# Performance work log

Measured on AMD Instinct MI355X. Metric: run time of the kernel, lower is better.

The kernel has to match this reference:

```python
import jax, jax.numpy as jnp
import numpy as np

EMBED = 8192      # DYNAMIC(2048) + STATIC(6144)
U0, U1 = 1024, 256  # units
EGO = 3
NUM_HEAD = 6
ACTION = 2
MEAN_SCALE = 5.0
INIT_STD = 5.0
MIN_STD = 1e-4
BATCH = 8192


def setup_inputs() -> dict:
    key = jax.random.key(0)
    ks = jax.random.split(key, 10)
    s = lambda fan_in: 1.0 / np.sqrt(fan_in)
    x = jax.random.normal(ks[0], (BATCH, EMBED), dtype=jnp.float32)
    # command head index in [0, 6) == RoadOption.value - 1
    command = jax.random.randint(ks[1], (BATCH,), 0, NUM_HEAD, dtype=jnp.int32)
    ego_state = jax.random.normal(ks[2], (BATCH, EGO), dtype=jnp.float32)
    # shared trunk fc: Linear(EMBED -> U0)
    fc_W = jax.random.uniform(ks[3], (EMBED, U0), jnp.float32, -s(EMBED), s(EMBED))
    fc_b = jax.random.uniform(ks[4], (U0,), jnp.float32, -s(EMBED), s(EMBED))
    # per-head MLP: Linear(U0+EGO -> U1) -> ReLU -> Linear(U1 -> 2*ACTION)
    cin = U0 + EGO
    W1 = jax.random.uniform(ks[5], (NUM_HEAD, cin, U1), jnp.float32, -s(cin), s(cin))
    b1 = jax.random.uniform(ks[6], (NUM_HEAD, U1), jnp.float32, -s(cin), s(cin))
    W2 = jax.random.uniform(ks[7], (NUM_HEAD, U1, 2 * ACTION), jnp.float32, -s(U1), s(U1))
    b2 = jax.random.uniform(ks[8], (NUM_HEAD, 2 * ACTION), jnp.float32, -s(U1), s(U1))
    return {"x": x, "command": command, "ego_state": ego_state,
            "fc_W": fc_W, "fc_b": fc_b, "W1": W1, "b1": b1, "W2": W2, "b2": b2}


def reference(x, command, ego_state, fc_W, fc_b, W1, b1, W2, b2):
    # shared trunk: Linear + ReLU, then concat ego state -> [B, U0+EGO]
    h = jax.nn.relu(x @ fc_W + fc_b)
    h = jnp.concatenate([h, ego_state], axis=-1)
    # routed heads: compute all 6 small heads densely, then select per sample
    # (faithful math; an optimized kernel would gather->grouped GEMM->scatter)
    h1 = jax.nn.relu(jnp.einsum('bi,hio->bho', h, W1) + b1)          # [B, H, U1]
    h2 = jnp.einsum('bhi,hio->bho', h1, W2) + b2                      # [B, H, 2A]
    sel = jnp.take_along_axis(h2, command[:, None, None].astype(jnp.int32), axis=1)
    out = sel[:, 0, :]                                                # [B, 2A]
    mean, std = jnp.split(out, 2, axis=-1)
    mean = MEAN_SCALE * jnp.tanh(mean / MEAN_SCALE)
    raw_init_std = np.float32(np.log(np.exp(INIT_STD) - 1.0))
    std = jax.nn.softplus(std + raw_init_std) + MIN_STD
    # distribution parameters (pre TanhBijector Normal params)
    return jnp.concatenate([mean, std], axis=-1)
```

## Files before the change

kernel.cpp:

```cpp
#include <hip/hip_runtime.h>
#include <stdint.h>

typedef short bf16x8 __attribute__((ext_vector_type(8)));
typedef float f32x4 __attribute__((ext_vector_type(4)));

#define BATCH 8192
#define EMBED 8192
#define U0    1024
#define U1    256
#define NHEAD 6

__device__ __forceinline__ unsigned short f2bf(float f) {
  union { float f; unsigned int u; } v; v.f = f;
  unsigned int u = v.u;
  unsigned int r = u + 0x7FFFu + ((u >> 16) & 1u);
  return (unsigned short)(r >> 16);
}
__device__ __forceinline__ unsigned int pk2(float lo, float hi) {
  return (unsigned int)f2bf(lo) | ((unsigned int)f2bf(hi) << 16);
}
__device__ __forceinline__ void async_copy16(const void* g, void* l) {
  __builtin_amdgcn_global_load_lds((const __attribute__((address_space(1))) void*)g,
                                   (__attribute__((address_space(3))) void*)l, 16, 0, 0);
}

__global__ void cvt_x_kernel(const float* __restrict__ x, unsigned short* __restrict__ xb) {
  long i = ((long)blockIdx.x * 256 + threadIdx.x) * 8;
  float4 a = *(const float4*)(x + i);
  float4 b = *(const float4*)(x + i + 4);
  uint4 r;
  r.x = pk2(a.x, a.y); r.y = pk2(a.z, a.w);
  r.z = pk2(b.x, b.y); r.w = pk2(b.z, b.w);
  *(uint4*)(xb + i) = r;
}

__global__ void transpose_cvt_kernel(const float* __restrict__ in, unsigned short* __restrict__ out,
                                     int R, int C, long in_z, long out_z) {
  __shared__ unsigned short tile[64][65];
  const float* inp = in + (long)blockIdx.z * in_z;
  unsigned short* outp = out + (long)blockIdx.z * out_z;
  int r0 = blockIdx.x * 64;
  int c0 = blockIdx.y * 64;
  int lc = threadIdx.x & 63;
  int lr = threadIdx.x >> 6;
#pragma unroll
  for (int i = 0; i < 16; i++) {
    int r = lr + i * 4;
    tile[r][lc] = f2bf(inp[(long)(r0 + r) * C + (c0 + lc)]);
  }
  __syncthreads();
#pragma unroll
  for (int i = 0; i < 16; i++) {
    int c = lr + i * 4;
    outp[(long)(c0 + c) * R + (r0 + lc)] = tile[lc][c];
  }
}

__global__ void bucket_kernel(const int* __restrict__ cmd, int* __restrict__ idxlist,
                              int* __restrict__ meta) {
  __shared__ int cnt[NHEAD], cur[NHEAD], off[NHEAD + 1];
  int tid = threadIdx.x;
  if (tid < NHEAD) cnt[tid] = 0;
  __syncthreads();
  for (int b = tid; b < BATCH; b += blockDim.x) atomicAdd(&cnt[cmd[b]], 1);
  __syncthreads();
  if (tid == 0) {
    int s = 0;
    for (int h2 = 0; h2 < NHEAD; h2++) { off[h2] = s; s += cnt[h2]; }
    off[NHEAD] = s;
  }
  __syncthreads();
  if (tid < NHEAD) cur[tid] = off[tid];
  if (tid <= NHEAD) meta[tid] = off[tid];
  __syncthreads();
  for (int b = tid; b < BATCH; b += blockDim.x) {
    int p = atomicAdd(&cur[cmd[b]], 1);
    idxlist[p] = b;
  }
}

__global__ __launch_bounds__(256) void gemm_kernel(const unsigned short* __restrict__ xb,
                                                   const unsigned short* __restrict__ wt,
                                                   const float* __restrict__ fc_b,
                                                   unsigned short* __restrict__ h) {
  __shared__ uint4 As[1024];
  __shared__ uint4 Bs[1024];
  int tid  = threadIdx.x;
  int lane = tid & 63;
  int wave = tid >> 6;
  int wm = wave >> 1, wn = wave & 1;
  int m0 = blockIdx.y * 128;
  int n0 = blockIdx.x * 128;
  int l15 = lane & 15, lq = lane >> 4;

  long asrc[4], bsrc[4];
#pragma unroll
  for (int j = 0; j < 4; j++) {
    int c = wave * 4 + j;
    int cwm = c >> 3, cks = (c >> 2) & 1, cmi = c & 3;
    int kofs = cks * 32 + lq * 8;
    asrc[j] = (long)(m0 + cwm * 64 + cmi * 16 + l15) * EMBED + kofs;
    bsrc[j] = (long)(n0 + cwm * 64 + cmi * 16 + l15) * EMBED + kofs;
  }

  f32x4 zero = {0.f, 0.f, 0.f, 0.f};
  f32x4 acc[4][4];
#pragma unroll
  for (int mi = 0; mi < 4; mi++)
#pragma unroll
    for (int ni = 0; ni < 4; ni++) acc[mi][ni] = zero;

  for (int k0 = 0; k0 < EMBED; k0 += 64) {
    __syncthreads();
#pragma unroll
    for (int j = 0; j < 4; j++) {
      int c = wave * 4 + j;
      async_copy16(xb + asrc[j] + k0, &As[c * 64 + lane]);
      async_copy16(wt + bsrc[j] + k0, &Bs[c * 64 + lane]);
    }
    __syncthreads();
#pragma unroll
    for (int ks = 0; ks < 2; ks++) {
      bf16x8 af[4], bfr[4];
#pragma unroll
      for (int mi = 0; mi < 4; mi++) af[mi] = *(const bf16x8*)&As[((wm * 2 + ks) * 4 + mi) * 64 + lane];
#pragma unroll
      for (int ni = 0; ni < 4; ni++) bfr[ni] = *(const bf16x8*)&Bs[((wn * 2 + ks) * 4 + ni) * 64 + lane];
#pragma unroll
      for (int mi = 0; mi < 4; mi++)
#pragma unroll
        for (int ni = 0; ni < 4; ni++)
          acc[mi][ni] = __builtin_amdgcn_mfma_f32_16x16x32_bf16(af[mi], bfr[ni], acc[mi][ni], 0, 0, 0);
    }
  }

#pragma unroll
  for (int ni = 0; ni < 4; ni++) {
    int col = n0 + wn * 64 + ni * 16 + l15;
    float bias = fc_b[col];
#pragma unroll
    for (int mi = 0; mi < 4; mi++) {
      int rbase = m0 + wm * 64 + mi * 16 + lq * 4;
#pragma unroll
      for (int r = 0; r < 4; r++) {
        float v = acc[mi][ni][r] + bias;
        v = v > 0.f ? v : 0.f;
        h[(long)(rbase + r) * U0 + col] = f2bf(v);
      }
    }
  }
}

__global__ __launch_bounds__(256) void head_kernel(const unsigned short* __restrict__ h,
                                                   const unsigned short* __restrict__ w1t,
                                                   const float* __restrict__ W1,
                                                   const float* __restrict__ b1,
                                                   const float* __restrict__ W2,
                                                   const float* __restrict__ b2,
                                                   const float* __restrict__ ego,
                                                   const int* __restrict__ idxlist,
                                                   const int* __restrict__ meta,
                                                   float* __restrict__ out) {
  int hd = blockIdx.y;
  int off = meta[hd];
  int cnt = meta[hd + 1] - off;
  int t0 = blockIdx.x * 32;
  if (t0 >= cnt) return;

  __shared__ int ridx[32];
  __shared__ float h1s[32][257];
  int tid = threadIdx.x;
  if (tid < 32) {
    int i = t0 + tid;
    ridx[tid] = idxlist[off + (i < cnt ? i : 0)];
  }
  __syncthreads();

  int lane = tid & 63, wave = tid >> 6;
  int l15 = lane & 15, lq = lane >> 4;

  long abase[2];
#pragma unroll
  for (int mi = 0; mi < 2; mi++) abase[mi] = (long)ridx[mi * 16 + l15] * U0 + lq * 8;
  long bbase[4];
#pragma unroll
  for (int ni = 0; ni < 4; ni++)
    bbase[ni] = (long)(hd * 256 + wave * 64 + ni * 16 + l15) * 1024 + lq * 8;

  f32x4 zero = {0.f, 0.f, 0.f, 0.f};
  f32x4 acc[2][4];
#pragma unroll
  for (int mi = 0; mi < 2; mi++)
#pragma unroll
    for (int ni = 0; ni < 4; ni++) acc[mi][ni] = zero;

#pragma unroll 2
  for (int k0 = 0; k0 < 1024; k0 += 32) {
    bf16x8 af[2], bfr[4];
#pragma unroll
    for (int mi = 0; mi < 2; mi++) af[mi] = *(const bf16x8*)(h + abase[mi] + k0);
#pragma unroll
    for (int ni = 0; ni < 4; ni++) bfr[ni] = *(const bf16x8*)(w1t + bbase[ni] + k0);
#pragma unroll
    for (int mi = 0; mi < 2; mi++)
#pragma unroll
      for (int ni = 0; ni < 4; ni++)
        acc[mi][ni] = __builtin_amdgcn_mfma_f32_16x16x32_bf16(af[mi], bfr[ni], acc[mi][ni], 0, 0, 0);
  }

  const float* W1e = W1 + (long)hd * 1027 * 256 + (long)1024 * 256;
#pragma unroll
  for (int mi = 0; mi < 2; mi++)
#pragma unroll
    for (int r = 0; r < 4; r++) {
      int rl = mi * 16 + lq * 4 + r;
      int b = ridx[rl];
      float e0 = ego[b * 3 + 0], e1 = ego[b * 3 + 1], e2 = ego[b * 3 + 2];
#pragma unroll
      for (int ni = 0; ni < 4; ni++) {
        int col = wave * 64 + ni * 16 + l15;
        float v = acc[mi][ni][r] + b1[hd * 256 + col]
                + e0 * W1e[col] + e1 * W1e[256 + col] + e2 * W1e[512 + col];
        h1s[rl][col] = v > 0.f ? v : 0.f;
      }
    }
  __syncthreads();

  if (tid < 128) {
    int t = tid >> 2, o2 = tid & 3;
    if (t0 + t < cnt) {
      const float* w2 = W2 + (long)hd * 256 * 4;
      float sum = b2[hd * 4 + o2];
      for (int i = 0; i < 256; i++) sum += h1s[t][i] * w2[i * 4 + o2];
      int b = ridx[t];
      float res;
      if (o2 < 2) {
        res = 5.0f * tanhf(sum * 0.2f);
      } else {
        float z = sum + 4.99323838f;
        res = (z > 20.f ? z : log1pf(expf(z))) + 1e-4f;
      }
      out[b * 4 + o2] = res;
    }
  }
}

extern "C" void kernel_launch(void* const* d_in, const int* in_sizes, int n_in,
                              void* d_out, int out_size, void* d_ws, size_t ws_size,
                              hipStream_t stream) {
  const float* x   = (const float*)d_in[0];
  const int*   cmd = (const int*)d_in[1];
  const float* ego = (const float*)d_in[2];
  const float* fcW = (const float*)d_in[3];
  const float* fcb = (const float*)d_in[4];
  const float* W1  = (const float*)d_in[5];
  const float* b1  = (const float*)d_in[6];
  const float* W2  = (const float*)d_in[7];
  const float* b2  = (const float*)d_in[8];
  float* out = (float*)d_out;

  char* ws = (char*)d_ws;
  unsigned short* xb   = (unsigned short*)(ws);
  unsigned short* wt   = (unsigned short*)(ws + 134217728);
  unsigned short* hbuf = (unsigned short*)(ws + 150994944);
  unsigned short* w1t  = (unsigned short*)(ws + 167772160);
  int* idxlist         = (int*)(ws + 170917888);
  int* meta            = (int*)(ws + 170950656);

  hipLaunchKernelGGL(cvt_x_kernel, dim3(32768), dim3(256), 0, stream, x, xb);
  hipLaunchKernelGGL(transpose_cvt_kernel, dim3(128, 16, 1), dim3(256), 0, stream,
                     fcW, wt, 8192, 1024, 0L, 0L);
  hipLaunchKernelGGL(transpose_cvt_kernel, dim3(16, 4, 6), dim3(256), 0, stream,
                     W1, w1t, 1024, 256, (long)1027 * 256, (long)256 * 1024);
  hipLaunchKernelGGL(bucket_kernel, dim3(1), dim3(1024), 0, stream, cmd, idxlist, meta);
  hipLaunchKernelGGL(gemm_kernel, dim3(8, 64), dim3(256), 0, stream, xb, wt, fcb, hbuf);
  hipLaunchKernelGGL(head_kernel, dim3(256, 6), dim3(256), 0, stream,
                     hbuf, w1t, W1, b1, W2, b2, ego, idxlist, meta, out);
}
```

Baseline: 757.2 us.

## Shrink GEMM N-tile to 64, reorder grid, and use wave-aggregated bucket atomics

The trunk GEMM tile changes from 128x128 to 128x64, which doubles the block count to 1024, halves the B shared-memory buffer, and adds a launch-bounds occupancy hint. The grid is reordered so blocks that share a weight N-slice run adjacently. The bucket kernel now uses wave ballots and popcount to do one shared atomic per wave per head instead of one per element. The smaller tile cuts per-block register and LDS use so more blocks fit per CU, at the cost of lower arithmetic intensity and more A-tile reloads.

```diff
diff --git a/kernel.cpp b/kernel.cpp
--- a/kernel.cpp
+++ b/kernel.cpp
@@ -60,9 +60,17 @@
                               int* __restrict__ meta) {
   __shared__ int cnt[NHEAD], cur[NHEAD], off[NHEAD + 1];
   int tid = threadIdx.x;
+  int lane = tid & 63;
   if (tid < NHEAD) cnt[tid] = 0;
   __syncthreads();
-  for (int b = tid; b < BATCH; b += blockDim.x) atomicAdd(&cnt[cmd[b]], 1);
+  for (int b = tid; b < BATCH; b += 1024) {
+    int c = cmd[b];
+#pragma unroll
+    for (int h2 = 0; h2 < NHEAD; h2++) {
+      unsigned long long m = __ballot(c == h2);
+      if (lane == 0 && m) atomicAdd(&cnt[h2], __popcll(m));
+    }
+  }
   __syncthreads();
   if (tid == 0) {
     int s = 0;
@@ -73,42 +81,55 @@
   if (tid < NHEAD) cur[tid] = off[tid];
   if (tid <= NHEAD) meta[tid] = off[tid];
   __syncthreads();
-  for (int b = tid; b < BATCH; b += blockDim.x) {
-    int p = atomicAdd(&cur[cmd[b]], 1);
-    idxlist[p] = b;
-  }
-}
-
-__global__ __launch_bounds__(256) void gemm_kernel(const unsigned short* __restrict__ xb,
-                                                   const unsigned short* __restrict__ wt,
-                                                   const float* __restrict__ fc_b,
-                                                   unsigned short* __restrict__ h) {
+  for (int b = tid; b < BATCH; b += 1024) {
+    int c = cmd[b];
+#pragma unroll
+    for (int h2 = 0; h2 < NHEAD; h2++) {
+      unsigned long long m = __ballot(c == h2);
+      int mypos = __popcll(m & ((1ull << lane) - 1ull));
+      int base = 0;
+      if (lane == 0 && m) base = atomicAdd(&cur[h2], __popcll(m));
+      base = __shfl(base, 0);
+      if (c == h2) idxlist[base + mypos] = b;
+    }
+  }
+}
+
+__global__ __launch_bounds__(256, 4) void gemm_kernel(const unsigned short* __restrict__ xb,
+                                                      const unsigned short* __restrict__ wt,
+                                                      const float* __restrict__ fc_b,
+                                                      unsigned short* __restrict__ h) {
   __shared__ uint4 As[1024];
-  __shared__ uint4 Bs[1024];
+  __shared__ uint4 Bs[512];
   int tid  = threadIdx.x;
   int lane = tid & 63;
   int wave = tid >> 6;
   int wm = wave >> 1, wn = wave & 1;
-  int m0 = blockIdx.y * 128;
-  int n0 = blockIdx.x * 128;
+  int m0 = blockIdx.x * 128;
+  int n0 = blockIdx.y * 64;
   int l15 = lane & 15, lq = lane >> 4;
 
-  long asrc[4], bsrc[4];
+  long asrc[4];
 #pragma unroll
   for (int j = 0; j < 4; j++) {
     int c = wave * 4 + j;
     int cwm = c >> 3, cks = (c >> 2) & 1, cmi = c & 3;
-    int kofs = cks * 32 + lq * 8;
-    asrc[j] = (long)(m0 + cwm * 64 + cmi * 16 + l15) * EMBED + kofs;
-    bsrc[j] = (long)(n0 + cwm * 64 + cmi * 16 + l15) * EMBED + kofs;
+    asrc[j] = (long)(m0 + cwm * 64 + cmi * 16 + l15) * EMBED + cks * 32 + lq * 8;
+  }
+  long bsrc[2];
+#pragma unroll
+  for (int j = 0; j < 2; j++) {
+    int c = wave * 2 + j;
+    int cwn = c >> 2, cks = (c >> 1) & 1, cni = c & 1;
+    bsrc[j] = (long)(n0 + cwn * 32 + cni * 16 + l15) * EMBED + cks * 32 + lq * 8;
   }
 
   f32x4 zero = {0.f, 0.f, 0.f, 0.f};
-  f32x4 acc[4][4];
+  f32x4 acc[4][2];
 #pragma unroll
   for (int mi = 0; mi < 4; mi++)
 #pragma unroll
-    for (int ni = 0; ni < 4; ni++) acc[mi][ni] = zero;
+    for (int ni = 0; ni < 2; ni++) acc[mi][ni] = zero;
 
   for (int k0 = 0; k0 < EMBED; k0 += 64) {
     __syncthreads();
@@ -116,27 +137,31 @@
     for (int j = 0; j < 4; j++) {
       int c = wave * 4 + j;
       async_copy16(xb + asrc[j] + k0, &As[c * 64 + lane]);
+    }
+#pragma unroll
+    for (int j = 0; j < 2; j++) {
+      int c = wave * 2 + j;
       async_copy16(wt + bsrc[j] + k0, &Bs[c * 64 + lane]);
     }
     __syncthreads();
 #pragma unroll
     for (int ks = 0; ks < 2; ks++) {
-      bf16x8 af[4], bfr[4];
+      bf16x8 af[4], bfr[2];
 #pragma unroll
       for (int mi = 0; mi < 4; mi++) af[mi] = *(const bf16x8*)&As[((wm * 2 + ks) * 4 + mi) * 64 + lane];
 #pragma unroll
-      for (int ni = 0; ni < 4; ni++) bfr[ni] = *(const bf16x8*)&Bs[((wn * 2 + ks) * 4 + ni) * 64 + lane];
+      for (int ni = 0; ni < 2; ni++) bfr[ni] = *(const bf16x8*)&Bs[((wn * 2 + ks) * 2 + ni) * 64 + lane];
 #pragma unroll
       for (int mi = 0; mi < 4; mi++)
 #pragma unroll
-        for (int ni = 0; ni < 4; ni++)
+        for (int ni = 0; ni < 2; ni++)
           acc[mi][ni] = __builtin_amdgcn_mfma_f32_16x16x32_bf16(af[mi], bfr[ni], acc[mi][ni], 0, 0, 0);
     }
   }
 
 #pragma unroll
-  for (int ni = 0; ni < 4; ni++) {
-    int col = n0 + wn * 64 + ni * 16 + l15;
+  for (int ni = 0; ni < 2; ni++) {
+    int col = n0 + wn * 32 + ni * 16 + l15;
     float bias = fc_b[col];
 #pragma unroll
     for (int mi = 0; mi < 4; mi++) {
@@ -273,7 +298,7 @@
   hipLaunchKernelGGL(transpose_cvt_kernel, dim3(16, 4, 6), dim3(256), 0, stream,
                      W1, w1t, 1024, 256, (long)1027 * 256, (long)256 * 1024);
   hipLaunchKernelGGL(bucket_kernel, dim3(1), dim3(1024), 0, stream, cmd, idxlist, meta);
-  hipLaunchKernelGGL(gemm_kernel, dim3(8, 64), dim3(256), 0, stream, xb, wt, fcb, hbuf);
+  hipLaunchKernelGGL(gemm_kernel, dim3(64, 16), dim3(256), 0, stream, xb, wt, fcb, hbuf);
   hipLaunchKernelGGL(head_kernel, dim3(256, 6), dim3(256), 0, stream,
                      hbuf, w1t, W1, b1, W2, b2, ego, idxlist, meta, out);
 }
```

New measurement: 895.6 us. 1.18x slower.

## Split trunk GEMM along K into two halves with a combine kernel

Applied to the files above, without the earlier changes.

Replaces the single trunk GEMM (512 blocks) with a split-K version over two K halves (1024 blocks), writing bf16 partial sums to a workspace. A separate combine kernel then adds the partials, the bias and the ReLU. The bucket kernel also switches to wave-level ballot and popcount aggregation to cut shared-memory atomics. The aim is more parallelism across CUs, at the cost of extra partial-sum traffic (32 MB), an extra launch, and bf16 rounding of the partials. The old path is kept as a fallback when the workspace is too small.

```diff
diff --git a/kernel.cpp b/kernel.cpp
--- a/kernel.cpp
+++ b/kernel.cpp
@@ -18,6 +18,12 @@
 }
 __device__ __forceinline__ unsigned int pk2(float lo, float hi) {
   return (unsigned int)f2bf(lo) | ((unsigned int)f2bf(hi) << 16);
+}
+__device__ __forceinline__ float bflo(unsigned int u) {
+  union { unsigned int u; float f; } v; v.u = u << 16; return v.f;
+}
+__device__ __forceinline__ float bfhi(unsigned int u) {
+  union { unsigned int u; float f; } v; v.u = u & 0xFFFF0000u; return v.f;
 }
 __device__ __forceinline__ void async_copy16(const void* g, void* l) {
   __builtin_amdgcn_global_load_lds((const __attribute__((address_space(1))) void*)g,
@@ -60,9 +66,17 @@
                               int* __restrict__ meta) {
   __shared__ int cnt[NHEAD], cur[NHEAD], off[NHEAD + 1];
   int tid = threadIdx.x;
+  int lane = tid & 63;
   if (tid < NHEAD) cnt[tid] = 0;
   __syncthreads();
-  for (int b = tid; b < BATCH; b += blockDim.x) atomicAdd(&cnt[cmd[b]], 1);
+  for (int b = tid; b < BATCH; b += 1024) {
+    int c = cmd[b];
+#pragma unroll
+    for (int h2 = 0; h2 < NHEAD; h2++) {
+      unsigned long long m = __ballot(c == h2);
+      if (lane == 0 && m) atomicAdd(&cnt[h2], __popcll(m));
+    }
+  }
   __syncthreads();
   if (tid == 0) {
     int s = 0;
@@ -73,10 +87,113 @@
   if (tid < NHEAD) cur[tid] = off[tid];
   if (tid <= NHEAD) meta[tid] = off[tid];
   __syncthreads();
-  for (int b = tid; b < BATCH; b += blockDim.x) {
-    int p = atomicAdd(&cur[cmd[b]], 1);
-    idxlist[p] = b;
-  }
+  for (int b = tid; b < BATCH; b += 1024) {
+    int c = cmd[b];
+#pragma unroll
+    for (int h2 = 0; h2 < NHEAD; h2++) {
+      unsigned long long m = __ballot(c == h2);
+      int mypos = __popcll(m & ((1ull << lane) - 1ull));
+      int base = 0;
+      if (lane == 0 && m) base = atomicAdd(&cur[h2], __popcll(m));
+      base = __shfl(base, 0);
+      if (c == h2) idxlist[base + mypos] = b;
+    }
+  }
+}
+
+__global__ __launch_bounds__(256, 4) void gemm_splitk_kernel(const unsigned short* __restrict__ xb,
+                                                             const unsigned short* __restrict__ wt,
+                                                             unsigned short* __restrict__ P) {
+  __shared__ uint4 As[1024];
+  __shared__ uint4 Bs[1024];
+  int tid  = threadIdx.x;
+  int lane = tid & 63;
+  int wave = tid >> 6;
+  int wm = wave >> 1, wn = wave & 1;
+  int m0 = blockIdx.x * 128;
+  int n0 = blockIdx.y * 128;
+  int kbase = blockIdx.z * (EMBED / 2);
+  unsigned short* pp = P + (long)blockIdx.z * BATCH * U0;
+  int l15 = lane & 15, lq = lane >> 4;
+
+  long asrc[4], bsrc[4];
+#pragma unroll
+  for (int j = 0; j < 4; j++) {
+    int c = wave * 4 + j;
+    int cwm = c >> 3, cks = (c >> 2) & 1, cmi = c & 3;
+    int kofs = kbase + cks * 32 + lq * 8;
+    asrc[j] = (long)(m0 + cwm * 64 + cmi * 16 + l15) * EMBED + kofs;
+    bsrc[j] = (long)(n0 + cwm * 64 + cmi * 16 + l15) * EMBED + kofs;
+  }
+
+  f32x4 zero = {0.f, 0.f, 0.f, 0.f};
+  f32x4 acc[4][4];
+#pragma unroll
+  for (int mi = 0; mi < 4; mi++)
+#pragma unroll
+    for (int ni = 0; ni < 4; ni++) acc[mi][ni] = zero;
+
+  for (int k0 = 0; k0 < EMBED / 2; k0 += 64) {
+    __syncthreads();
+#pragma unroll
+    for (int j = 0; j < 4; j++) {
+      int c = wave * 4 + j;
+      async_copy16(xb + asrc[j] + k0, &As[c * 64 + lane]);
+      async_copy16(wt + bsrc[j] + k0, &Bs[c * 64 + lane]);
+    }
+    __syncthreads();
+#pragma unroll
+    for (int ks = 0; ks < 2; ks++) {
+      bf16x8 af[4], bfr[4];
+#pragma unroll
+      for (int mi = 0; mi < 4; mi++) af[mi] = *(const bf16x8*)&As[((wm * 2 + ks) * 4 + mi) * 64 + lane];
+#pragma unroll
+      for (int ni = 0; ni < 4; ni++) bfr[ni] = *(const bf16x8*)&Bs[((wn * 2 + ks) * 4 + ni) * 64 + lane];
+#pragma unroll
+      for (int mi = 0; mi < 4; mi++)
+#pragma unroll
+        for (int ni = 0; ni < 4; ni++)
+          acc[mi][ni] = __builtin_amdgcn_mfma_f32_16x16x32_bf16(af[mi], bfr[ni], acc[mi][ni], 0, 0, 0);
+    }
+  }
+
+#pragma unroll
+  for (int ni = 0; ni < 4; ni++) {
+    int col = n0 + wn * 64 + ni * 16 + l15;
+#pragma unroll
+    for (int mi = 0; mi < 4; mi++) {
+      int rbase = m0 + wm * 64 + mi * 16 + lq * 4;
+#pragma unroll
+      for (int r = 0; r < 4; r++)
+        pp[(long)(rbase + r) * U0 + col] = f2bf(acc[mi][ni][r]);
+    }
+  }
+}
+
+__global__ void combine_kernel(const unsigned short* __restrict__ P,
+                               const float* __restrict__ fc_b,
+                               unsigned short* __restrict__ h) {
+  long i = ((long)blockIdx.x * 256 + threadIdx.x) * 8;
+  uint4 a = *(const uint4*)(P + i);
+  uint4 b = *(const uint4*)(P + (long)BATCH * U0 + i);
+  int col = (int)(i & (U0 - 1));
+  float4 b0 = *(const float4*)(fc_b + col);
+  float4 b1 = *(const float4*)(fc_b + col + 4);
+  float v0 = bflo(a.x) + bflo(b.x) + b0.x;
+  float v1 = bfhi(a.x) + bfhi(b.x) + b0.y;
+  float v2 = bflo(a.y) + bflo(b.y) + b0.z;
+  float v3 = bfhi(a.y) + bfhi(b.y) + b0.w;
+  float v4 = bflo(a.z) + bflo(b.z) + b1.x;
+  float v5 = bfhi(a.z) + bfhi(b.z) + b1.y;
+  float v6 = bflo(a.w) + bflo(b.w) + b1.z;
+  float v7 = bfhi(a.w) + bfhi(b.w) + b1.w;
+  v0 = v0 > 0.f ? v0 : 0.f;  v1 = v1 > 0.f ? v1 : 0.f;
+  v2 = v2 > 0.f ? v2 : 0.f;  v3 = v3 > 0.f ? v3 : 0.f;
+  v4 = v4 > 0.f ? v4 : 0.f;  v5 = v5 > 0.f ? v5 : 0.f;
+  v6 = v6 > 0.f ? v6 : 0.f;  v7 = v7 > 0.f ? v7 : 0.f;
+  uint4 r;
+  r.x = pk2(v0, v1); r.y = pk2(v2, v3); r.z = pk2(v4, v5); r.w = pk2(v6, v7);
+  *(uint4*)(h + i) = r;
 }
 
 __global__ __launch_bounds__(256) void gemm_kernel(const unsigned short* __restrict__ xb,
@@ -266,6 +383,8 @@
   unsigned short* w1t  = (unsigned short*)(ws + 167772160);
   int* idxlist         = (int*)(ws + 170917888);
   int* meta            = (int*)(ws + 170950656);
+  unsigned short* P    = (unsigned short*)(ws + 171048960);
+  const size_t ws_needed = 171048960ull + 2ull * BATCH * U0 * 2ull;
 
   hipLaunchKernelGGL(cvt_x_kernel, dim3(32768), dim3(256), 0, stream, x, xb);
   hipLaunchKernelGGL(transpose_cvt_kernel, dim3(128, 16, 1), dim3(256), 0, stream,
@@ -273,7 +392,12 @@
   hipLaunchKernelGGL(transpose_cvt_kernel, dim3(16, 4, 6), dim3(256), 0, stream,
                      W1, w1t, 1024, 256, (long)1027 * 256, (long)256 * 1024);
   hipLaunchKernelGGL(bucket_kernel, dim3(1), dim3(1024), 0, stream, cmd, idxlist, meta);
-  hipLaunchKernelGGL(gemm_kernel, dim3(8, 64), dim3(256), 0, stream, xb, wt, fcb, hbuf);
+  if (ws_size >= ws_needed) {
+    hipLaunchKernelGGL(gemm_splitk_kernel, dim3(64, 8, 2), dim3(256), 0, stream, xb, wt, P);
+    hipLaunchKernelGGL(combine_kernel, dim3(4096), dim3(256), 0, stream, P, fcb, hbuf);
+  } else {
+    hipLaunchKernelGGL(gemm_kernel, dim3(8, 64), dim3(256), 0, stream, xb, wt, fcb, hbuf);
+  }
   hipLaunchKernelGGL(head_kernel, dim3(256, 6), dim3(256), 0, stream,
                      hbuf, w1t, W1, b1, W2, b2, ego, idxlist, meta, out);
 }
```

Result: slower. 782.8 us (+3.4%).
